# Kernel optimization log

Hardware: AMD Instinct MI355X
Metric: run time of the kernel (lower is better)

The kernel has to match this reference:

```python
import jax, jax.numpy as jnp
import numpy as np

B_SZ, C_IN, H, W = 2, 96, 128, 128
DT_RANK, D_STATE, D_INNER = 8, 16, 96


def pscan2d(A, X):
    """Faithful port of PScan2DUnified.forward / pscan2d_optimized.

    A, X: (b, H, W, d, N). The source's downsweep writes into index_select
    COPIES (discarded in torch), so the effective computation is the upsweep
    only: at level k (stride s=2**k), for each 2x2 block of active elements,
    X[dst] += A[dst] * X[src]; A[dst] *= A[src], where src=(s-1::2s, s-1::2s)
    and dst=(2s-1::2s, 2s-1::2s). Requires H, W powers of two.
    """
    h, w = A.shape[1], A.shape[2]
    K = min(int(np.log2(h)), int(np.log2(w)))
    for k in range(K):
        s = 2 ** k
        Asrc = A[:, s - 1::2 * s, s - 1::2 * s]
        Xsrc = X[:, s - 1::2 * s, s - 1::2 * s]
        Adst = A[:, 2 * s - 1::2 * s, 2 * s - 1::2 * s]
        X = X.at[:, 2 * s - 1::2 * s, 2 * s - 1::2 * s].add(Adst * Xsrc)
        A = A.at[:, 2 * s - 1::2 * s, 2 * s - 1::2 * s].multiply(Asrc)
    return X


def setup_inputs() -> dict:
    key = jax.random.key(0)
    ks = jax.random.split(key, 5)
    x = jax.random.normal(ks[0], (B_SZ, C_IN, H, W), dtype=jnp.float32)
    # 1x1 conv weights stored as (out, in) matrices
    deltaBC_w = jax.random.normal(ks[1], (DT_RANK + 2 * D_STATE, C_IN), dtype=jnp.float32) * 0.02
    deltaBC_b = jnp.zeros((DT_RANK + 2 * D_STATE,), dtype=jnp.float32)
    dt_w = jax.random.normal(ks[2], (D_INNER, DT_RANK), dtype=jnp.float32) * 0.02
    dt_b = jnp.zeros((D_INNER,), dtype=jnp.float32)
    # faithful init: log(linspace(1,2,N)) repeated over d_inner
    A_log = jnp.tile(jnp.log(jnp.linspace(1.0, 2.0, D_STATE, dtype=jnp.float32)), (D_INNER, 1))
    D = jnp.ones((D_INNER,), dtype=jnp.float32)
    return {"x": x, "deltaBC_w": deltaBC_w, "deltaBC_b": deltaBC_b,
            "dt_w": dt_w, "dt_b": dt_b, "A_log": A_log, "D": D}


def reference(x, deltaBC_w, deltaBC_b, dt_w, dt_b, A_log, D):
    A = -jnp.exp(A_log)  # (d, N)
    # 1x1 conv == per-pixel matmul
    dBC = jnp.einsum('bchw,oc->bohw', x, deltaBC_w) + deltaBC_b[None, :, None, None]
    delta = dBC[:, :DT_RANK]
    Bm = dBC[:, DT_RANK:DT_RANK + D_STATE]
    Cm = dBC[:, DT_RANK + D_STATE:]
    delta = jax.nn.softplus(jnp.einsum('bchw,oc->bohw', delta, dt_w) + dt_b[None, :, None, None])
    delta = delta.transpose(0, 2, 3, 1)   # (b,H,W,d)
    Bm = Bm.transpose(0, 2, 3, 1)         # (b,H,W,N)
    Cm = Cm.transpose(0, 2, 3, 1)         # (b,H,W,N)
    xh = x.transpose(0, 2, 3, 1)          # (b,H,W,d)
    A_bar = jnp.exp(delta[..., None] * A)                         # (b,H,W,d,N)
    BX = (delta[..., None] * Bm[:, :, :, None, :]) * xh[..., None]  # (b,H,W,d,N)
    hs = pscan2d(A_bar, BX)                                       # (b,H,W,d,N)
    y = jnp.einsum('bhwdn,bhwn->bhwd', hs, Cm) + D * xh
    return y
```

## Files before the change

kernel.cpp:

```cpp
#include <hip/hip_runtime.h>
#include <cstdint>

#define CIN 96
#define DIN 96
#define DTR 8
#define DST 16
#define HH 128
#define WW 128
#define HW (HH*WW)
#define NPIX (2*HW)
#define LOG2E 1.4426950408889634f
#define NDIAG 63
#define DSLOT 128

__device__ __forceinline__ float softplus_f(float t) {
    return (t > 20.0f) ? t : __logf(1.0f + __expf(t));
}

__device__ __forceinline__ void load_An(const float* __restrict__ AwsT, int d, float* An) {
    float4 A0 = *reinterpret_cast<const float4*>(AwsT + d * 16);
    float4 A1 = *reinterpret_cast<const float4*>(AwsT + d * 16 + 4);
    float4 A2 = *reinterpret_cast<const float4*>(AwsT + d * 16 + 8);
    float4 A3 = *reinterpret_cast<const float4*>(AwsT + d * 16 + 12);
    An[0]=A0.x; An[1]=A0.y; An[2]=A0.z; An[3]=A0.w;
    An[4]=A1.x; An[5]=A1.y; An[6]=A1.z; An[7]=A1.w;
    An[8]=A2.x; An[9]=A2.y; An[10]=A2.z; An[11]=A2.w;
    An[12]=A3.x; An[13]=A3.y; An[14]=A3.z; An[15]=A3.w;
}

__device__ __forceinline__ float c_dot(const float* __restrict__ rc, const float* acc16) {
    float4 C0 = *reinterpret_cast<const float4*>(rc);
    float4 C1 = *reinterpret_cast<const float4*>(rc + 4);
    float4 C2 = *reinterpret_cast<const float4*>(rc + 8);
    float4 C3 = *reinterpret_cast<const float4*>(rc + 12);
    float ys = 0.f;
    ys = fmaf(acc16[0],C0.x,ys); ys = fmaf(acc16[1],C0.y,ys);
    ys = fmaf(acc16[2],C0.z,ys); ys = fmaf(acc16[3],C0.w,ys);
    ys = fmaf(acc16[4],C1.x,ys); ys = fmaf(acc16[5],C1.y,ys);
    ys = fmaf(acc16[6],C1.z,ys); ys = fmaf(acc16[7],C1.w,ys);
    ys = fmaf(acc16[8],C2.x,ys); ys = fmaf(acc16[9],C2.y,ys);
    ys = fmaf(acc16[10],C2.z,ys); ys = fmaf(acc16[11],C2.w,ys);
    ys = fmaf(acc16[12],C3.x,ys); ys = fmaf(acc16[13],C3.y,ys);
    ys = fmaf(acc16[14],C3.z,ys); ys = fmaf(acc16[15],C3.w,ys);
    return ys;
}

__global__ __launch_bounds__(512) void ssm2d_dbc(
    const float* __restrict__ x,
    const float* __restrict__ W1, const float* __restrict__ b1,
    const float* __restrict__ dtw, const float* __restrict__ dtb,
    const float* __restrict__ alog, const float* __restrict__ Dv,
    float* __restrict__ bc, float2* __restrict__ dc,
    float* __restrict__ Aws, float* __restrict__ out)
{
    __shared__ float sX[CIN][65];
    __shared__ float sOut[64][41];
    __shared__ float sDelta[DIN][65];
    __shared__ float sAn[DIN][17];
    __shared__ float sBC[64];

    const int t = threadIdx.x;
    const int blk = blockIdx.x;
    const int b = blk >> 8;
    const int tile = blk & 255;
    const int a = tile >> 2;
    const int b2 = tile & 3;
    const int r0 = a << 1;
    const int c0 = b2 << 5;
    const float* xb = x + (size_t)b * CIN * HW;

    #pragma unroll
    for (int it = 0; it < 3; ++it) {
        int i4 = it * 512 + t;
        int ch = i4 >> 4;
        int px4 = (i4 & 15) << 2;
        int row = r0 + (px4 >> 5);
        int col = c0 + (px4 & 31);
        float4 v = *reinterpret_cast<const float4*>(xb + (size_t)ch * HW + row * WW + col);
        sX[ch][px4 + 0] = v.x; sX[ch][px4 + 1] = v.y;
        sX[ch][px4 + 2] = v.z; sX[ch][px4 + 3] = v.w;
    }
    for (int i = t; i < DIN * DST; i += 512) {
        float v = -__expf(alog[i]) * LOG2E;
        sAn[i >> 4][i & 15] = v;
        if (blk == 0) Aws[i] = v;
    }
    __syncthreads();

    const int lane = t & 63;
    const int w = __builtin_amdgcn_readfirstlane(t >> 6);
    const int og = w * 5;
    float a0 = b1[og + 0], a1 = b1[og + 1], a2 = b1[og + 2],
          a3 = b1[og + 3], a4 = b1[og + 4];
    #pragma unroll 16
    for (int ch = 0; ch < CIN; ++ch) {
        float xv = sX[ch][lane];
        a0 = fmaf(xv, W1[(og + 0) * CIN + ch], a0);
        a1 = fmaf(xv, W1[(og + 1) * CIN + ch], a1);
        a2 = fmaf(xv, W1[(og + 2) * CIN + ch], a2);
        a3 = fmaf(xv, W1[(og + 3) * CIN + ch], a3);
        a4 = fmaf(xv, W1[(og + 4) * CIN + ch], a4);
    }
    sOut[lane][og + 0] = a0; sOut[lane][og + 1] = a1; sOut[lane][og + 2] = a2;
    sOut[lane][og + 3] = a3; sOut[lane][og + 4] = a4;
    __syncthreads();

    if (t < 64) {
        float s = 0.f;
        #pragma unroll
        for (int n = 0; n < DST; ++n) s += sOut[t][8 + n] * sOut[t][24 + n];
        sBC[t] = s;
    }
    __syncthreads();

    #pragma unroll
    for (int it = 0; it < 12; ++it) {
        int i = it * 512 + t;
        int px = i / 96;
        int d = i - px * 96;
        float tt = dtb[d];
        float4 wA = *reinterpret_cast<const float4*>(dtw + d * DTR);
        float4 wB = *reinterpret_cast<const float4*>(dtw + d * DTR + 4);
        tt = fmaf(sOut[px][0], wA.x, tt); tt = fmaf(sOut[px][1], wA.y, tt);
        tt = fmaf(sOut[px][2], wA.z, tt); tt = fmaf(sOut[px][3], wA.w, tt);
        tt = fmaf(sOut[px][4], wB.x, tt); tt = fmaf(sOut[px][5], wB.y, tt);
        tt = fmaf(sOut[px][6], wB.z, tt); tt = fmaf(sOut[px][7], wB.w, tt);
        float delta = softplus_f(tt);
        float xv = sX[d][px];
        sDelta[d][px] = delta;
        int rg = r0 + (px >> 5), cg = c0 + (px & 31);
        size_t pg = (size_t)b * HW + rg * WW + cg;
        out[pg * 96 + d] = xv * fmaf(delta, sBC[px], Dv[d]);
        if (((rg - cg) & 3) == 0) {
            int td = ((rg - cg) >> 2) + 31;
            int jd = (rg < cg) ? rg : cg;
            size_t row = (size_t)(b * NDIAG + td) * DSLOT + jd;
            dc[row * 96 + d] = make_float2(delta, delta * xv);
        }
    }
    #pragma unroll
    for (int it = 0; it < 4; ++it) {
        int i = it * 512 + t;
        int px = i >> 5;
        int n = i & 31;
        int rg = r0 + (px >> 5), cg = c0 + (px & 31);
        if (((rg - cg) & 3) == 0) {
            int td = ((rg - cg) >> 2) + 31;
            int jd = (rg < cg) ? rg : cg;
            size_t row = (size_t)(b * NDIAG + td) * DSLOT + jd;
            bc[row * 32 + n] = sOut[px][8 + n];
        }
    }
    __syncthreads();

    for (int ii = t; ii < 16 * 96; ii += 512) {
        int k = ii / 96;
        int d = ii - k * 96;
        bool live = !((a & 1) && (k & 1));
        int pxd = 33 + 2 * k;
        int anc = 2 * k;
        float ddst = sDelta[d][pxd];
        float ca = sDelta[d][anc] * sX[d][anc];
        float y = 0.f;
        #pragma unroll
        for (int n = 0; n < 16; ++n)
            y = fmaf(sOut[pxd][24 + n] * exp2f(sAn[d][n] * ddst) * sOut[anc][8 + n], ca, y);
        if (live) {
            int rg = r0 + 1, cg = c0 + 1 + 2 * k;
            size_t g = ((size_t)b * HW + rg * WW + cg) * 96 + d;
            out[g] += y;
        }
    }
}

template<int M>
__device__ __forceinline__ void decode_item(int e, size_t& obase, size_t& drow,
                                            int& d, bool& live) {
    d = e % 96;
    int pxi = e / 96;
    const int sh = 7 - M;
    const int nM = 1 << sh;
    const int half = nM * nM;
    int img = pxi >= half;
    int e2 = pxi - (img ? half : 0);
    int rr = e2 >> sh;
    int cc = e2 & (nM - 1);
    live = ((rr & cc & 1) == 0);
    int r = ((rr + 1) << M) - 1;
    int c = ((cc + 1) << M) - 1;
    obase = ((size_t)(img * HW + r * WW + c)) * 96 + d;
    int td = ((r - c) >> 2) + 31;
    int jd = (r < c) ? r : c;
    drow = (size_t)(img * NDIAG + td) * DSLOT + jd;
}

template<int L>
__device__ __forceinline__ void chain_LT(size_t obase, size_t drow, int d, bool live,
    const float* __restrict__ bc, const float2* __restrict__ dc,
    const float* __restrict__ AwsT, float* __restrict__ out)
{
    float2 v0 = dc[drow * 96 + d];
    float2 vj[L - 1];
    #pragma unroll
    for (int j = 1; j < L; ++j)
        vj[j - 1] = dc[(drow - j) * 96 + d];
    float An[16];
    load_An(AwsT, d, An);
    float acc16[16];
    #pragma unroll
    for (int n = 0; n < 16; ++n) acc16[n] = 0.f;
    float S = v0.x;
    #pragma unroll
    for (int j = 1; j < L; ++j) {
        const float* rb = bc + (drow - j) * 32;
        float4 B0 = *reinterpret_cast<const float4*>(rb);
        float4 B1 = *reinterpret_cast<const float4*>(rb + 4);
        float4 B2 = *reinterpret_cast<const float4*>(rb + 8);
        float4 B3 = *reinterpret_cast<const float4*>(rb + 12);
        float Bv[16] = {B0.x,B0.y,B0.z,B0.w, B1.x,B1.y,B1.z,B1.w,
                        B2.x,B2.y,B2.z,B2.w, B3.x,B3.y,B3.z,B3.w};
        float cj = vj[j - 1].y;
        #pragma unroll
        for (int n = 0; n < 16; ++n)
            acc16[n] = fmaf(exp2f(An[n] * S) * Bv[n], cj, acc16[n]);
        S += vj[j - 1].x;
    }
    float ys = c_dot(bc + drow * 32 + 16, acc16);
    if (live) out[obase] += ys;
}

__device__ __forceinline__ void chain_RT(size_t obase, size_t drow, int d, int L, bool live,
    const float* __restrict__ bc, const float2* __restrict__ dc,
    const float* __restrict__ AwsT, float* __restrict__ out)
{
    float An[16];
    load_An(AwsT, d, An);
    float acc16[16];
    #pragma unroll
    for (int n = 0; n < 16; ++n) acc16[n] = 0.f;
    float S = dc[drow * 96 + d].x;
    for (int j = 1; j < L; ++j) {
        float2 v = dc[(drow - j) * 96 + d];
        const float* rb = bc + (drow - j) * 32;
        float4 B0 = *reinterpret_cast<const float4*>(rb);
        float4 B1 = *reinterpret_cast<const float4*>(rb + 4);
        float4 B2 = *reinterpret_cast<const float4*>(rb + 8);
        float4 B3 = *reinterpret_cast<const float4*>(rb + 12);
        float Bv[16] = {B0.x,B0.y,B0.z,B0.w, B1.x,B1.y,B1.z,B1.w,
                        B2.x,B2.y,B2.z,B2.w, B3.x,B3.y,B3.z,B3.w};
        #pragma unroll
        for (int n = 0; n < 16; ++n)
            acc16[n] = fmaf(exp2f(An[n] * S) * Bv[n], v.y, acc16[n]);
        S += v.x;
    }
    float ys = c_dot(bc + drow * 32 + 16, acc16);
    if (live) out[obase] += ys;
}

#define K2_M2 768
#define K2_M3 192
#define K2_M4 48
#define K2_LONG 768
__global__ __launch_bounds__(256) void ssm2d_scan(
    const float* __restrict__ bc, const float2* __restrict__ dc,
    const float* __restrict__ AwsT, float* __restrict__ out)
{
    const int t = threadIdx.x;
    const int blk = blockIdx.x;

    if (blk < K2_M2) {
        int e = blk * 256 + t;
        size_t obase, drow; int d; bool live;
        decode_item<2>(e, obase, drow, d, live);
        chain_LT<4>(obase, drow, d, live, bc, dc, AwsT, out);
    } else if (blk < K2_M2 + K2_M3) {
        int e = (blk - K2_M2) * 256 + t;
        size_t obase, drow; int d; bool live;
        decode_item<3>(e, obase, drow, d, live);
        chain_RT(obase, drow, d, 8, live, bc, dc, AwsT, out);
    } else if (blk < K2_M2 + K2_M3 + K2_M4) {
        int e = (blk - K2_M2 - K2_M3) * 256 + t;
        size_t obase, drow; int d; bool live;
        decode_item<4>(e, obase, drow, d, live);
        chain_RT(obase, drow, d, 16, live, bc, dc, AwsT, out);
    } else {
        const int wv = t >> 6;
        const int lane = t & 63;
        int waveid = (blk - (K2_M2 + K2_M3 + K2_M4)) * 4 + wv;
        int pix = waveid / DIN;
        int d = waveid - pix * DIN;
        int batch = pix >> 4;
        int sel = pix & 15;
        int r = ((sel >> 2) + 1) * 32 - 1;
        int c = ((sel & 3) + 1) * 32 - 1;
        int p = batch * HW + r * WW + c;
        int m = __builtin_ctz(r + 1);
        int mc = __builtin_ctz(c + 1);
        if (mc < m) m = mc;
        int L = 1 << m;

        int td = ((r - c) >> 2) + 31;
        int jd = (r < c) ? r : c;
        size_t drow = (size_t)(batch * NDIAG + td) * DSLOT + jd;

        float An[16];
        load_An(AwsT, d, An);
        float acc16[16];
        #pragma unroll
        for (int n = 0; n < 16; ++n) acc16[n] = 0.0f;
        float Scarry = 0.0f;

        for (int jb = 0; jb < L; jb += 64) {
            int j = jb + lane;
            bool act = (j < L);
            int jc = act ? j : 0;
            size_t prow = drow - jc;
            float2 v = dc[prow * 96 + d];
            float dj = act ? v.x : 0.0f;
            float cj = (j >= 1 && act) ? v.y : 0.0f;

            float incl = dj;
            #pragma unroll
            for (int off = 1; off < 64; off <<= 1) {
                float u = __shfl_up(incl, off);
                if (lane >= off) incl += u;
            }
            float S = Scarry + incl - dj;

            const float* rb = bc + prow * 32;
            float4 B0 = *reinterpret_cast<const float4*>(rb);
            float4 B1 = *reinterpret_cast<const float4*>(rb + 4);
            float4 B2 = *reinterpret_cast<const float4*>(rb + 8);
            float4 B3 = *reinterpret_cast<const float4*>(rb + 12);
            float Bv[16] = {B0.x,B0.y,B0.z,B0.w, B1.x,B1.y,B1.z,B1.w,
                            B2.x,B2.y,B2.z,B2.w, B3.x,B3.y,B3.z,B3.w};
            #pragma unroll
            for (int n = 0; n < 16; ++n)
                acc16[n] = fmaf(exp2f(An[n] * S) * Bv[n], cj, acc16[n]);

            Scarry += __shfl(incl, 63);
        }

        #pragma unroll
        for (int off = 32; off >= 1; off >>= 1) {
            #pragma unroll
            for (int n = 0; n < 16; ++n) acc16[n] += __shfl_xor(acc16[n], off);
        }

        if (lane == 0) {
            float y = c_dot(bc + drow * 32 + 16, acc16);
            out[(size_t)p * 96 + d] += y;
        }
    }
}

extern "C" void kernel_launch(void* const* d_in, const int* in_sizes, int n_in,
                              void* d_out, int out_size, void* d_ws, size_t ws_size,
                              hipStream_t stream) {
    const float* x    = (const float*)d_in[0];
    const float* W1   = (const float*)d_in[1];
    const float* b1   = (const float*)d_in[2];
    const float* dtw  = (const float*)d_in[3];
    const float* dtb  = (const float*)d_in[4];
    const float* alog = (const float*)d_in[5];
    const float* Dv   = (const float*)d_in[6];
    float* out = (float*)d_out;

    char* ws = (char*)d_ws;
    float2* dc  = (float2*)(ws);
    float*  bcb = (float*)(ws + 12582912);
    float*  Aws = (float*)(ws + 14680064);

    hipLaunchKernelGGL(ssm2d_dbc, dim3(512), dim3(512), 0, stream,
                       x, W1, b1, dtw, dtb, alog, Dv,
                       bcb, dc, Aws, out);
    hipLaunchKernelGGL(ssm2d_scan, dim3(K2_M2 + K2_M3 + K2_M4 + K2_LONG), dim3(256), 0, stream,
                       bcb, dc, Aws, out);
}
```

Before: 37.10 us.

## Recompute delta in scan kernel from stored dt-rank projections instead of storing delta

The first kernel no longer writes a per-channel (delta, delta*x) float2 buffer. It writes only delta*x per channel plus the 8 dt-rank values per diagonal pixel. The scan kernel recomputes delta with an 8-term dot product and softplus from those values and dt_w/dt_b. This roughly halves the per-channel intermediate traffic, paid for with extra ALU work and transcendental calls in the scan chains.

```diff
diff --git a/kernel.cpp b/kernel.cpp
--- a/kernel.cpp
+++ b/kernel.cpp
@@ -15,6 +15,16 @@
 
 __device__ __forceinline__ float softplus_f(float t) {
     return (t > 20.0f) ? t : __logf(1.0f + __expf(t));
+}
+
+__device__ __forceinline__ float delta_of(const float4 k0, const float4 k1,
+                                          const float4 wA, const float4 wB, float tb) {
+    float tt = tb;
+    tt = fmaf(k0.x, wA.x, tt); tt = fmaf(k0.y, wA.y, tt);
+    tt = fmaf(k0.z, wA.z, tt); tt = fmaf(k0.w, wA.w, tt);
+    tt = fmaf(k1.x, wB.x, tt); tt = fmaf(k1.y, wB.y, tt);
+    tt = fmaf(k1.z, wB.z, tt); tt = fmaf(k1.w, wB.w, tt);
+    return softplus_f(tt);
 }
 
 __device__ __forceinline__ void load_An(const float* __restrict__ AwsT, int d, float* An) {
@@ -50,7 +60,7 @@
     const float* __restrict__ W1, const float* __restrict__ b1,
     const float* __restrict__ dtw, const float* __restrict__ dtb,
     const float* __restrict__ alog, const float* __restrict__ Dv,
-    float* __restrict__ bc, float2* __restrict__ dc,
+    float* __restrict__ bc, float* __restrict__ dx, float* __restrict__ kw,
     float* __restrict__ Aws, float* __restrict__ out)
 {
     __shared__ float sX[CIN][65];
@@ -135,7 +145,7 @@
             int td = ((rg - cg) >> 2) + 31;
             int jd = (rg < cg) ? rg : cg;
             size_t row = (size_t)(b * NDIAG + td) * DSLOT + jd;
-            dc[row * 96 + d] = make_float2(delta, delta * xv);
+            dx[row * 96 + d] = delta * xv;
         }
     }
     #pragma unroll
@@ -149,6 +159,17 @@
             int jd = (rg < cg) ? rg : cg;
             size_t row = (size_t)(b * NDIAG + td) * DSLOT + jd;
             bc[row * 32 + n] = sOut[px][8 + n];
+        }
+    }
+    {
+        int px = t >> 3;
+        int o = t & 7;
+        int rg = r0 + (px >> 5), cg = c0 + (px & 31);
+        if (((rg - cg) & 3) == 0) {
+            int td = ((rg - cg) >> 2) + 31;
+            int jd = (rg < cg) ? rg : cg;
+            size_t row = (size_t)(b * NDIAG + td) * DSLOT + jd;
+            kw[row * 8 + o] = sOut[px][o];
         }
     }
     __syncthreads();
@@ -196,20 +217,33 @@
 
 template<int L>
 __device__ __forceinline__ void chain_LT(size_t obase, size_t drow, int d, bool live,
-    const float* __restrict__ bc, const float2* __restrict__ dc,
-    const float* __restrict__ AwsT, float* __restrict__ out)
+    const float* __restrict__ bc, const float* __restrict__ dx,
+    const float* __restrict__ kw, const float* __restrict__ dtw,
+    const float* __restrict__ dtb, const float* __restrict__ AwsT,
+    float* __restrict__ out)
 {
-    float2 v0 = dc[drow * 96 + d];
-    float2 vj[L - 1];
-    #pragma unroll
-    for (int j = 1; j < L; ++j)
-        vj[j - 1] = dc[(drow - j) * 96 + d];
+    float4 wA = *reinterpret_cast<const float4*>(dtw + d * DTR);
+    float4 wB = *reinterpret_cast<const float4*>(dtw + d * DTR + 4);
+    float tb = dtb[d];
+    float4 kr0[L], kr1[L];
+    float dxv[L];
+    #pragma unroll
+    for (int j = 0; j < L; ++j) {
+        const float* kr = kw + (drow - j) * 8;
+        kr0[j] = *reinterpret_cast<const float4*>(kr);
+        kr1[j] = *reinterpret_cast<const float4*>(kr + 4);
+        dxv[j] = dx[(drow - j) * 96 + d];
+    }
+    float del[L];
+    #pragma unroll
+    for (int j = 0; j < L; ++j)
+        del[j] = delta_of(kr0[j], kr1[j], wA, wB, tb);
     float An[16];
     load_An(AwsT, d, An);
     float acc16[16];
     #pragma unroll
     for (int n = 0; n < 16; ++n) acc16[n] = 0.f;
-    float S = v0.x;
+    float S = del[0];
     #pragma unroll
     for (int j = 1; j < L; ++j) {
         const float* rb = bc + (drow - j) * 32;
@@ -219,29 +253,40 @@
         float4 B3 = *reinterpret_cast<const float4*>(rb + 12);
         float Bv[16] = {B0.x,B0.y,B0.z,B0.w, B1.x,B1.y,B1.z,B1.w,
                         B2.x,B2.y,B2.z,B2.w, B3.x,B3.y,B3.z,B3.w};
-        float cj = vj[j - 1].y;
+        float cj = dxv[j];
         #pragma unroll
         for (int n = 0; n < 16; ++n)
             acc16[n] = fmaf(exp2f(An[n] * S) * Bv[n], cj, acc16[n]);
-        S += vj[j - 1].x;
+        S += del[j];
     }
     float ys = c_dot(bc + drow * 32 + 16, acc16);
     if (live) out[obase] += ys;
 }
 
 __device__ __forceinline__ void chain_RT(size_t obase, size_t drow, int d, int L, bool live,
-    const float* __restrict__ bc, const float2* __restrict__ dc,
-    const float* __restrict__ AwsT, float* __restrict__ out)
+    const float* __restrict__ bc, const float* __restrict__ dx,
+    const float* __restrict__ kw, const float* __restrict__ dtw,
+    const float* __restrict__ dtb, const float* __restrict__ AwsT,
+    float* __restrict__ out)
 {
+    float4 wA = *reinterpret_cast<const float4*>(dtw + d * DTR);
+    float4 wB = *reinterpret_cast<const float4*>(dtw + d * DTR + 4);
+    float tb = dtb[d];
     float An[16];
     load_An(AwsT, d, An);
     float acc16[16];
     #pragma unroll
     for (int n = 0; n < 16; ++n) acc16[n] = 0.f;
-    float S = dc[drow * 96 + d].x;
+    const float* kr = kw + drow * 8;
+    float S = delta_of(*reinterpret_cast<const float4*>(kr),
+                       *reinterpret_cast<const float4*>(kr + 4), wA, wB, tb);
     for (int j = 1; j < L; ++j) {
-        float2 v = dc[(drow - j) * 96 + d];
-        const float* rb = bc + (drow - j) * 32;
+        size_t row = drow - j;
+        const float* krj = kw + row * 8;
+        float dj = delta_of(*reinterpret_cast<const float4*>(krj),
+                            *reinterpret_cast<const float4*>(krj + 4), wA, wB, tb);
+        float cj = dx[row * 96 + d];
+        const float* rb = bc + row * 32;
         float4 B0 = *reinterpret_cast<const float4*>(rb);
         float4 B1 = *reinterpret_cast<const float4*>(rb + 4);
         float4 B2 = *reinterpret_cast<const float4*>(rb + 8);
@@ -250,8 +295,8 @@
                         B2.x,B2.y,B2.z,B2.w, B3.x,B3.y,B3.z,B3.w};
         #pragma unroll
         for (int n = 0; n < 16; ++n)
-            acc16[n] = fmaf(exp2f(An[n] * S) * Bv[n], v.y, acc16[n]);
-        S += v.x;
+            acc16[n] = fmaf(exp2f(An[n] * S) * Bv[n], cj, acc16[n]);
+        S += dj;
     }
     float ys = c_dot(bc + drow * 32 + 16, acc16);
     if (live) out[obase] += ys;
@@ -262,8 +307,10 @@
 #define K2_M4 48
 #define K2_LONG 768
 __global__ __launch_bounds__(256) void ssm2d_scan(
-    const float* __restrict__ bc, const float2* __restrict__ dc,
-    const float* __restrict__ AwsT, float* __restrict__ out)
+    const float* __restrict__ bc, const float* __restrict__ dx,
+    const float* __restrict__ kw, const float* __restrict__ dtw,
+    const float* __restrict__ dtb, const float* __restrict__ AwsT,
+    float* __restrict__ out)
 {
     const int t = threadIdx.x;
     const int blk = blockIdx.x;
@@ -272,17 +319,17 @@
         int e = blk * 256 + t;
         size_t obase, drow; int d; bool live;
         decode_item<2>(e, obase, drow, d, live);
-        chain_LT<4>(obase, drow, d, live, bc, dc, AwsT, out);
+        chain_LT<4>(obase, drow, d, live, bc, dx, kw, dtw, dtb, AwsT, out);
     } else if (blk < K2_M2 + K2_M3) {
         int e = (blk - K2_M2) * 256 + t;
         size_t obase, drow; int d; bool live;
         decode_item<3>(e, obase, drow, d, live);
-        chain_RT(obase, drow, d, 8, live, bc, dc, AwsT, out);
+        chain_RT(obase, drow, d, 8, live, bc, dx, kw, dtw, dtb, AwsT, out);
     } else if (blk < K2_M2 + K2_M3 + K2_M4) {
         int e = (blk - K2_M2 - K2_M3) * 256 + t;
         size_t obase, drow; int d; bool live;
         decode_item<4>(e, obase, drow, d, live);
-        chain_RT(obase, drow, d, 16, live, bc, dc, AwsT, out);
+        chain_RT(obase, drow, d, 16, live, bc, dx, kw, dtw, dtb, AwsT, out);
     } else {
         const int wv = t >> 6;
         const int lane = t & 63;
@@ -303,6 +350,9 @@
         int jd = (r < c) ? r : c;
         size_t drow = (size_t)(batch * NDIAG + td) * DSLOT + jd;
 
+        float4 wA = *reinterpret_cast<const float4*>(dtw + d * DTR);
+        float4 wB = *reinterpret_cast<const float4*>(dtw + d * DTR + 4);
+        float tb = dtb[d];
         float An[16];
         load_An(AwsT, d, An);
         float acc16[16];
@@ -315,9 +365,11 @@
             bool act = (j < L);
             int jc = act ? j : 0;
             size_t prow = drow - jc;
-            float2 v = dc[prow * 96 + d];
-            float dj = act ? v.x : 0.0f;
-            float cj = (j >= 1 && act) ? v.y : 0.0f;
+            const float* krj = kw + prow * 8;
+            float dj = delta_of(*reinterpret_cast<const float4*>(krj),
+                                *reinterpret_cast<const float4*>(krj + 4), wA, wB, tb);
+            if (!act) dj = 0.0f;
+            float cj = (j >= 1 && act) ? dx[prow * 96 + d] : 0.0f;
 
             float incl = dj;
             #pragma unroll
@@ -367,13 +419,14 @@
     float* out = (float*)d_out;
 
     char* ws = (char*)d_ws;
-    float2* dc  = (float2*)(ws);
-    float*  bcb = (float*)(ws + 12582912);
-    float*  Aws = (float*)(ws + 14680064);
+    float* dx  = (float*)(ws);
+    float* kw  = (float*)(ws + 6291456);
+    float* bcb = (float*)(ws + 6815744);
+    float* Aws = (float*)(ws + 8912896);
 
     hipLaunchKernelGGL(ssm2d_dbc, dim3(512), dim3(512), 0, stream,
                        x, W1, b1, dtw, dtb, alog, Dv,
-                       bcb, dc, Aws, out);
+                       bcb, dx, kw, Aws, out);
     hipLaunchKernelGGL(ssm2d_scan, dim3(K2_M2 + K2_M3 + K2_M4 + K2_LONG), dim3(256), 0, stream,
-                       bcb, dc, Aws, out);
-}
+                       bcb, dx, kw, dtw, dtb, Aws, out);
+}
```

Result: no change. 37.05 us (-0.1%).
